# Performance work log

Hardware: AMD Instinct MI355X
Metric: run time of the kernel (lower is better)

The kernel has to match this reference:

```python
import jax, jax.numpy as jnp
import numpy as np

DIM = 192
K_LARGE = 21
K_SMALL = 5
EPS = 1e-5
DN = ('NCHW', 'OIHW', 'NCHW')


def depthwise_conv(x, w, k):
    pad = k // 2
    return jax.lax.conv_general_dilated(
        x, w, window_strides=(1, 1), padding=[(pad, pad), (pad, pad)],
        dimension_numbers=DN, feature_group_count=DIM)


def setup_inputs() -> dict:
    key = jax.random.key(0)
    ks = jax.random.split(key, 7)
    x = jax.random.normal(ks[0], (16, DIM, 56, 56), dtype=jnp.float32)
    w_large = jax.random.normal(ks[1], (DIM, 1, K_LARGE, K_LARGE), dtype=jnp.float32) * 0.05
    w_small = jax.random.normal(ks[2], (DIM, 1, K_SMALL, K_SMALL), dtype=jnp.float32) * 0.1
    gamma = jnp.ones((DIM,), dtype=jnp.float32)
    beta = jnp.zeros((DIM,), dtype=jnp.float32)
    w_pw = jax.random.normal(ks[3], (DIM, DIM, 1, 1), dtype=jnp.float32) * 0.05
    b_pw = jnp.zeros((DIM,), dtype=jnp.float32)
    return {"x": x, "w_large": w_large, "w_small": w_small,
            "gamma": gamma, "beta": beta, "w_pw": w_pw, "b_pw": b_pw}


def reference(x, w_large, w_small, gamma, beta, w_pw, b_pw):
    identity = x
    out = depthwise_conv(x, w_large, K_LARGE) + depthwise_conv(x, w_small, K_SMALL)
    # GroupNorm with 1 group: normalize over (C,H,W) per sample
    mean = jnp.mean(out, axis=(1, 2, 3), keepdims=True)
    var = jnp.var(out, axis=(1, 2, 3), keepdims=True)
    out = (out - mean) * jax.lax.rsqrt(var + EPS)
    out = out * gamma[None, :, None, None] + beta[None, :, None, None]
    out = jax.nn.gelu(out, approximate=False)  # torch nn.GELU default is exact
    # 1x1 pointwise conv with bias
    out = jax.lax.conv_general_dilated(
        out, w_pw, window_strides=(1, 1), padding='VALID', dimension_numbers=DN)
    out = out + b_pw[None, :, None, None]
    return out + identity
```

## Files before the change

### kernel.cpp

```cpp
#include <hip/hip_runtime.h>
#include <math.h>

#define DIM 192
#define HW 56
#define NPIX 3136
#define NSAMP 16
#define GN_EPS 1e-5f

typedef float f32x2 __attribute__((ext_vector_type(2)));
typedef float f32x4 __attribute__((ext_vector_type(4)));
typedef float f32x16 __attribute__((ext_vector_type(16)));
typedef unsigned int u32x4 __attribute__((ext_vector_type(4)));
typedef _Float16 h2 __attribute__((ext_vector_type(2)));
typedef _Float16 h8 __attribute__((ext_vector_type(8)));
typedef __bf16 bf16x8 __attribute__((ext_vector_type(8)));

#define WS_OFF_PARTIALS 38535168
#define WS_OFF_STATS    38559744
#define WS_OFF_WB       38559872

__device__ __forceinline__ unsigned int pack_h2(float a, float b) {
    h2 h;
    h[0] = (_Float16)a;
    h[1] = (_Float16)b;
    return __builtin_bit_cast(unsigned int, h);
}

__global__ void conv_w_kernel(const float* __restrict__ w, __bf16* __restrict__ wb) {
    int i = blockIdx.x * 256 + threadIdx.x;
    if (i < DIM * DIM) wb[i] = (__bf16)w[i];
}

#define S2(PH, t) ((((PH) - (t)) % 21 + 21) % 21)
#define AB16(a, b) __builtin_amdgcn_alignbit((a), (b), 16)

#define RING_Q(rg, dd, PH, QMAX) do { \
    rg[S2(PH,0)] += dd[0]; \
    rg[S2(PH,1)] += dd[1]; \
    rg[S2(PH,2)] += dd[2]; \
    rg[S2(PH,3)] += dd[3]; \
    if (12 <= (QMAX)) rg[S2(PH,8)]  += dd[4]; else rg[S2(PH,8)]  += hi ? 0.f : dd[4]; \
    if (13 <= (QMAX)) rg[S2(PH,9)]  += dd[5]; else rg[S2(PH,9)]  += hi ? 0.f : dd[5]; \
    if (14 <= (QMAX)) rg[S2(PH,10)] += dd[6]; else rg[S2(PH,10)] += hi ? 0.f : dd[6]; \
    if (15 <= (QMAX)) rg[S2(PH,11)] += dd[7]; \
    else if (11 <= (QMAX)) rg[S2(PH,11)] += hi ? 0.f : dd[7]; \
    if (20 <= (QMAX)) rg[S2(PH,16)] += dd[8]; \
    else if (16 <= (QMAX)) rg[S2(PH,16)] += hi ? 0.f : dd[8]; \
    if (17 <= (QMAX)) rg[S2(PH,17)] += hi ? 0.f : dd[9]; \
    rg[S2(PH,4)] += hi ? dd[9] : 0.f; \
    if (18 <= (QMAX)) rg[S2(PH,18)] += hi ? 0.f : dd[10]; \
    rg[S2(PH,5)] += hi ? dd[10] : 0.f; \
    if (19 <= (QMAX)) rg[S2(PH,19)] += hi ? 0.f : dd[11]; \
    rg[S2(PH,6)] += hi ? dd[11] : 0.f; \
    if (11 <= (QMAX)) rg[S2(PH,11)] += hi ? 0.f : dd[12]; \
    if (12 <= (QMAX)) rg[S2(PH,12)] += hi ? 0.f : dd[13]; \
} while (0)

#define STEP(PH_, QMAX_, RVAL_) do { \
    const unsigned int* rp = base + ((RVAL_) - 10) * 48; \
    unsigned int d0 = rp[0], d1 = rp[1], d2 = rp[2], d3 = rp[3], d4 = rp[4]; \
    unsigned int e0 = rp[8], e1 = rp[9], e2 = rp[10], e3 = rp[11], e4 = rp[12]; \
    { \
        u32x4 q0; q0[0] = d0; q0[1] = d1; q0[2] = d2; q0[3] = d3; \
        u32x4 q1; q1[0] = e0; q1[1] = e1; q1[2] = e2; q1[3] = e3; \
        f32x16 acc = __builtin_amdgcn_mfma_f32_32x32x16_f16( \
            A0, __builtin_bit_cast(h8, q0), CZ, 0, 0, 0); \
        acc = __builtin_amdgcn_mfma_f32_32x32x16_f16( \
            A1, __builtin_bit_cast(h8, q1), acc, 0, 0, 0); \
        RING_Q(ring0, acc, PH_, QMAX_); \
    } \
    { \
        u32x4 q0, q1; \
        q0[0] = AB16(d1, d0); q0[1] = AB16(d2, d1); q0[2] = AB16(d3, d2); q0[3] = AB16(d4, d3); \
        q1[0] = AB16(e1, e0); q1[1] = AB16(e2, e1); q1[2] = AB16(e3, e2); q1[3] = AB16(e4, e3); \
        f32x16 acc = __builtin_amdgcn_mfma_f32_32x32x16_f16( \
            A0, __builtin_bit_cast(h8, q0), CZ, 0, 0, 0); \
        acc = __builtin_amdgcn_mfma_f32_32x32x16_f16( \
            A1, __builtin_bit_cast(h8, q1), acc, 0, 0, 0); \
        RING_Q(ring1, acc, PH_, QMAX_); \
    } \
} while (0)

#define EMIT(PH_, RVAL_) do { \
    const int s0 = S2(PH_, 20), s1 = S2(PH_, 16); \
    float p0 = hi ? ring0[s1] : ring0[s0]; \
    float p1 = hi ? ring1[s1] : ring1[s0]; \
    ring0[s0] = hi ? ring0[s0] : 0.f; \
    ring0[s1] = hi ? 0.f : ring0[s1]; \
    ring1[s0] = hi ? ring1[s0] : 0.f; \
    ring1[s1] = hi ? 0.f : ring1[s1]; \
    float t0 = p0 + __shfl_xor(p0, 32); \
    float t1 = p1 + __shfl_xor(p1, 32); \
    if (!hi && nok) { \
        const int y = (RVAL_) - 20; \
        f32x2 st; st[0] = t0; st[1] = t1; \
        *(f32x2*)(top + y * HW + 2 * n) = st; \
        lsum += t0 + t1; \
        lss += t0 * t0 + t1 * t1; \
    } \
} while (0)

__global__ __launch_bounds__(64, 3)
void dwconv_kernel(const float* __restrict__ x,
                   const float* __restrict__ wl,
                   const float* __restrict__ wsm,
                   float* __restrict__ tmp,
                   float* __restrict__ partials) {
    __shared__ unsigned int tile[56 * 48];

    const int plane = blockIdx.x;
    const int ch = plane % DIM;
    const int l = threadIdx.x;
    const int n = l & 31;
    const int h = l >> 5;
    const bool hi = (h == 1);
    const bool nok = (n < 28);
    const float* xp = x + (size_t)plane * NPIX;

    {
        u32x4* t4 = (u32x4*)tile;
        for (int i = l; i < 672; i += 64) {
            u32x4 z; z[0] = 0; z[1] = 0; z[2] = 0; z[3] = 0;
            t4[i] = z;
        }
    }
    __syncthreads();
    for (int i = l; i < 56 * 28; i += 64) {
        int row = i / 28, j = i - row * 28;
        f32x2 v = *(const f32x2*)(xp + row * HW + 2 * j);
        tile[row * 48 + 5 + j] = pack_h2(v[0], v[1]);
    }

    h8 A0, A1;
    {
        const int m = n;
        #pragma unroll
        for (int e = 0; e < 8; ++e) {
            int tp = 8 * h + e;
            float v0 = 0.f, v1 = 0.f;
            if (m <= 20) {
                if (tp <= 20) v0 = wl[ch * 441 + m * 21 + tp];
                int tq = tp + 16;
                if (tq <= 20) v1 = wl[ch * 441 + m * 21 + tq];
            } else if (m <= 25 && tp >= 8 && tp <= 12) {
                v0 = wsm[ch * 25 + (m - 21) * 5 + (tp - 8)];
            }
            A0[e] = (_Float16)v0;
            A1[e] = (_Float16)v1;
        }
    }
    __syncthreads();

    float ring0[21], ring1[21];
    #pragma unroll
    for (int s = 0; s < 21; ++s) { ring0[s] = 0.f; ring1[s] = 0.f; }
    f32x16 CZ;
    #pragma unroll
    for (int s = 0; s < 16; ++s) CZ[s] = 0.f;

    float lsum = 0.f, lss = 0.f;
    float* top = tmp + (size_t)plane * NPIX;
    const unsigned int* base = tile + (n + 4 * h);

    #pragma unroll
    for (int rr = 0; rr < 10; ++rr) {
        STEP(10 + rr, 10 + rr, 10 + rr);
    }
    for (int bb = 0; bb < 3; ++bb) {
        #pragma unroll
        for (int u = 0; u < 21; ++u) {
            const int r = 20 + 21 * bb + u;
            if (r > 75) continue;
            if (r < 66) {
                STEP(20 + u, 20, r);
            }
            EMIT(20 + u, r);
        }
    }

    #pragma unroll
    for (int off = 32; off > 0; off >>= 1) {
        lsum += __shfl_down(lsum, off);
        lss  += __shfl_down(lss, off);
    }
    if (l == 0) {
        partials[2 * plane + 0] = lsum;
        partials[2 * plane + 1] = lss;
    }
}

__global__ void stats_kernel(const float* __restrict__ partials, float* __restrict__ stats) {
    const int n = blockIdx.x;
    const int t = threadIdx.x;
    float s = 0.f, ss = 0.f;
    for (int c = t; c < DIM; c += 64) {
        s  += partials[2 * (n * DIM + c) + 0];
        ss += partials[2 * (n * DIM + c) + 1];
    }
    #pragma unroll
    for (int off = 32; off > 0; off >>= 1) {
        s  += __shfl_down(s, off);
        ss += __shfl_down(ss, off);
    }
    if (t == 0) {
        const float inv = 1.f / 602112.f;
        float mean = s * inv;
        float var = ss * inv - mean * mean;
        stats[2 * n + 0] = mean;
        stats[2 * n + 1] = rsqrtf(var + GN_EPS);
    }
}

__device__ __forceinline__ float fast_gelu(float y) {
    float z = fabsf(y) * 0.70710678118654752f;
    float tt = __builtin_amdgcn_rcpf(1.f + 0.3275911f * z);
    float poly = tt * (0.254829592f + tt * (-0.284496736f + tt * (1.421413741f
               + tt * (-1.453152027f + tt * 1.061405429f))));
    float er = 1.f - poly * __expf(-z * z);
    er = copysignf(er, y);
    return 0.5f * y * (1.f + er);
}

__global__ __launch_bounds__(192)
void pw_kernel(const float* __restrict__ tmp, const float* __restrict__ x,
               const float* __restrict__ gamma, const float* __restrict__ beta,
               const __bf16* __restrict__ wb, const float* __restrict__ bpw,
               const float* __restrict__ stats, float* __restrict__ out) {
    __shared__ __bf16 g_lds[32 * 200];

    const int bid = blockIdx.x;
    const int n = bid / 98;
    const int pt = bid - n * 98;
    const int px0 = pt * 32;
    const int t = threadIdx.x;

    const float mean = stats[2 * n + 0];
    const float rstd = stats[2 * n + 1];

    {
        const float a = rstd * gamma[t];
        const float b = beta[t] - mean * a;
        const float* tp = tmp + ((size_t)n * DIM + t) * NPIX + px0;
        #pragma unroll
        for (int k = 0; k < 8; ++k) {
            f32x4 v = *(const f32x4*)(tp + 4 * k);
            #pragma unroll
            for (int j = 0; j < 4; ++j) {
                float y = v[j] * a + b;
                g_lds[(4 * k + j) * 200 + t] = (__bf16)fast_gelu(y);
            }
        }
    }
    __syncthreads();

    const int w = t >> 6;
    const int l = t & 63;
    const int lane16 = l & 15, lg = l >> 4;

    f32x4 acc[2][4];
    #pragma unroll
    for (int p = 0; p < 2; ++p)
        #pragma unroll
        for (int m = 0; m < 4; ++m) { acc[p][m][0]=0.f; acc[p][m][1]=0.f; acc[p][m][2]=0.f; acc[p][m][3]=0.f; }

    const char* gbase = (const char*)g_lds;
    #pragma unroll
    for (int kk = 0; kk < 6; ++kk) {
        const int k0 = 32 * kk;
        bf16x8 bf0 = *(const bf16x8*)(gbase + lane16 * 400 + (k0 + 8 * lg) * 2);
        bf16x8 bf1 = *(const bf16x8*)(gbase + (16 + lane16) * 400 + (k0 + 8 * lg) * 2);
        #pragma unroll
        for (int m = 0; m < 4; ++m) {
            const int co = 64 * w + 16 * m + lane16;
            bf16x8 af = *(const bf16x8*)(wb + co * DIM + k0 + 8 * lg);
            acc[0][m] = __builtin_amdgcn_mfma_f32_16x16x32_bf16(af, bf0, acc[0][m], 0, 0, 0);
            acc[1][m] = __builtin_amdgcn_mfma_f32_16x16x32_bf16(af, bf1, acc[1][m], 0, 0, 0);
        }
    }

    const float* xb = x + (size_t)n * DIM * NPIX;
    float* ob = out + (size_t)n * DIM * NPIX;
    #pragma unroll
    for (int m = 0; m < 4; ++m) {
        f32x4 b4 = *(const f32x4*)(bpw + 64 * w + 16 * m + 4 * lg);
        #pragma unroll
        for (int p = 0; p < 2; ++p)
            #pragma unroll
            for (int j = 0; j < 4; ++j) {
                const int co = 64 * w + 16 * m + 4 * lg + j;
                const int idx = co * NPIX + px0 + p * 16 + lane16;
                ob[idx] = acc[p][m][j] + b4[j] + xb[idx];
            }
    }
}

extern "C" void kernel_launch(void* const* d_in, const int* in_sizes, int n_in,
                              void* d_out, int out_size, void* d_ws, size_t ws_size,
                              hipStream_t stream) {
    (void)in_sizes; (void)n_in; (void)out_size; (void)ws_size;
    const float* x     = (const float*)d_in[0];
    const float* wl    = (const float*)d_in[1];
    const float* wsm   = (const float*)d_in[2];
    const float* gamma = (const float*)d_in[3];
    const float* beta  = (const float*)d_in[4];
    const float* wpw   = (const float*)d_in[5];
    const float* bpw   = (const float*)d_in[6];
    float* out = (float*)d_out;

    char* wsb = (char*)d_ws;
    float* tmp      = (float*)wsb;
    float* partials = (float*)(wsb + WS_OFF_PARTIALS);
    float* stats    = (float*)(wsb + WS_OFF_STATS);
    __bf16* wb      = (__bf16*)(wsb + WS_OFF_WB);

    conv_w_kernel<<<144, 256, 0, stream>>>(wpw, wb);
    dwconv_kernel<<<NSAMP * DIM, 64, 0, stream>>>(x, wl, wsm, tmp, partials);
    stats_kernel<<<NSAMP, 64, 0, stream>>>(partials, stats);
    pw_kernel<<<NSAMP * 98, 192, 0, stream>>>(tmp, x, gamma, beta, wb, bpw, stats, out);
}
```

Before: 114.4 us.

## Vectorize LDS tile loads, use mask multiplies, pkrtz packing, relax launch bounds

Measured after the change: 126.4 us. +10.5%, slower.

```diff
diff --git a/kernel.cpp b/kernel.cpp
--- a/kernel.cpp
+++ b/kernel.cpp
@@ -13,6 +13,7 @@
 typedef unsigned int u32x4 __attribute__((ext_vector_type(4)));
 typedef _Float16 h2 __attribute__((ext_vector_type(2)));
 typedef _Float16 h8 __attribute__((ext_vector_type(8)));
+typedef __fp16 fp16x2 __attribute__((ext_vector_type(2)));
 typedef __bf16 bf16x8 __attribute__((ext_vector_type(8)));
 
 #define WS_OFF_PARTIALS 38535168
@@ -20,10 +21,8 @@
 #define WS_OFF_WB       38559872
 
 __device__ __forceinline__ unsigned int pack_h2(float a, float b) {
-    h2 h;
-    h[0] = (_Float16)a;
-    h[1] = (_Float16)b;
-    return __builtin_bit_cast(unsigned int, h);
+    fp16x2 r = __builtin_amdgcn_cvt_pkrtz(a, b);
+    return __builtin_bit_cast(unsigned int, r);
 }
 
 __global__ void conv_w_kernel(const float* __restrict__ w, __bf16* __restrict__ wb) {
@@ -39,40 +38,41 @@
     rg[S2(PH,1)] += dd[1]; \
     rg[S2(PH,2)] += dd[2]; \
     rg[S2(PH,3)] += dd[3]; \
-    if (12 <= (QMAX)) rg[S2(PH,8)]  += dd[4]; else rg[S2(PH,8)]  += hi ? 0.f : dd[4]; \
-    if (13 <= (QMAX)) rg[S2(PH,9)]  += dd[5]; else rg[S2(PH,9)]  += hi ? 0.f : dd[5]; \
-    if (14 <= (QMAX)) rg[S2(PH,10)] += dd[6]; else rg[S2(PH,10)] += hi ? 0.f : dd[6]; \
+    if (12 <= (QMAX)) rg[S2(PH,8)]  += dd[4];  else rg[S2(PH,8)]  += mlo * dd[4]; \
+    if (13 <= (QMAX)) rg[S2(PH,9)]  += dd[5];  else rg[S2(PH,9)]  += mlo * dd[5]; \
+    if (14 <= (QMAX)) rg[S2(PH,10)] += dd[6];  else rg[S2(PH,10)] += mlo * dd[6]; \
     if (15 <= (QMAX)) rg[S2(PH,11)] += dd[7]; \
-    else if (11 <= (QMAX)) rg[S2(PH,11)] += hi ? 0.f : dd[7]; \
+    else if (11 <= (QMAX)) rg[S2(PH,11)] += mlo * dd[7]; \
     if (20 <= (QMAX)) rg[S2(PH,16)] += dd[8]; \
-    else if (16 <= (QMAX)) rg[S2(PH,16)] += hi ? 0.f : dd[8]; \
-    if (17 <= (QMAX)) rg[S2(PH,17)] += hi ? 0.f : dd[9]; \
-    rg[S2(PH,4)] += hi ? dd[9] : 0.f; \
-    if (18 <= (QMAX)) rg[S2(PH,18)] += hi ? 0.f : dd[10]; \
-    rg[S2(PH,5)] += hi ? dd[10] : 0.f; \
-    if (19 <= (QMAX)) rg[S2(PH,19)] += hi ? 0.f : dd[11]; \
-    rg[S2(PH,6)] += hi ? dd[11] : 0.f; \
-    if (11 <= (QMAX)) rg[S2(PH,11)] += hi ? 0.f : dd[12]; \
-    if (12 <= (QMAX)) rg[S2(PH,12)] += hi ? 0.f : dd[13]; \
+    else if (16 <= (QMAX)) rg[S2(PH,16)] += mlo * dd[8]; \
+    if (17 <= (QMAX)) rg[S2(PH,17)] += mlo * dd[9]; \
+    rg[S2(PH,4)] += mhi * dd[9]; \
+    if (18 <= (QMAX)) rg[S2(PH,18)] += mlo * dd[10]; \
+    rg[S2(PH,5)] += mhi * dd[10]; \
+    if (19 <= (QMAX)) rg[S2(PH,19)] += mlo * dd[11]; \
+    rg[S2(PH,6)] += mhi * dd[11]; \
+    if (11 <= (QMAX)) rg[S2(PH,11)] += mlo * dd[12]; \
+    if (12 <= (QMAX)) rg[S2(PH,12)] += mlo * dd[13]; \
 } while (0)
 
 #define STEP(PH_, QMAX_, RVAL_) do { \
     const unsigned int* rp = base + ((RVAL_) - 10) * 48; \
-    unsigned int d0 = rp[0], d1 = rp[1], d2 = rp[2], d3 = rp[3], d4 = rp[4]; \
-    unsigned int e0 = rp[8], e1 = rp[9], e2 = rp[10], e3 = rp[11], e4 = rp[12]; \
+    u32x4 dq = *(const u32x4*)rp; \
+    unsigned int d4 = rp[4]; \
+    u32x4 eq = *(const u32x4*)(rp + 8); \
     { \
-        u32x4 q0; q0[0] = d0; q0[1] = d1; q0[2] = d2; q0[3] = d3; \
-        u32x4 q1; q1[0] = e0; q1[1] = e1; q1[2] = e2; q1[3] = e3; \
         f32x16 acc = __builtin_amdgcn_mfma_f32_32x32x16_f16( \
-            A0, __builtin_bit_cast(h8, q0), CZ, 0, 0, 0); \
+            A0, __builtin_bit_cast(h8, dq), CZ, 0, 0, 0); \
         acc = __builtin_amdgcn_mfma_f32_32x32x16_f16( \
-            A1, __builtin_bit_cast(h8, q1), acc, 0, 0, 0); \
+            A1, __builtin_bit_cast(h8, eq), acc, 0, 0, 0); \
         RING_Q(ring0, acc, PH_, QMAX_); \
     } \
     { \
         u32x4 q0, q1; \
-        q0[0] = AB16(d1, d0); q0[1] = AB16(d2, d1); q0[2] = AB16(d3, d2); q0[3] = AB16(d4, d3); \
-        q1[0] = AB16(e1, e0); q1[1] = AB16(e2, e1); q1[2] = AB16(e3, e2); q1[3] = AB16(e4, e3); \
+        q0[0] = AB16(dq[1], dq[0]); q0[1] = AB16(dq[2], dq[1]); \
+        q0[2] = AB16(dq[3], dq[2]); q0[3] = AB16(d4, dq[3]); \
+        q1[0] = AB16(eq[1], eq[0]); q1[1] = AB16(eq[2], eq[1]); \
+        q1[2] = AB16(eq[3], eq[2]); q1[3] = q1[2];  \
         f32x16 acc = __builtin_amdgcn_mfma_f32_32x32x16_f16( \
             A0, __builtin_bit_cast(h8, q0), CZ, 0, 0, 0); \
         acc = __builtin_amdgcn_mfma_f32_32x32x16_f16( \
@@ -85,10 +85,10 @@
     const int s0 = S2(PH_, 20), s1 = S2(PH_, 16); \
     float p0 = hi ? ring0[s1] : ring0[s0]; \
     float p1 = hi ? ring1[s1] : ring1[s0]; \
-    ring0[s0] = hi ? ring0[s0] : 0.f; \
-    ring0[s1] = hi ? 0.f : ring0[s1]; \
-    ring1[s0] = hi ? ring1[s0] : 0.f; \
-    ring1[s1] = hi ? 0.f : ring1[s1]; \
+    ring0[s0] *= mhi;   \
+    ring0[s1] *= mlo;   \
+    ring1[s0] *= mhi; \
+    ring1[s1] *= mlo; \
     float t0 = p0 + __shfl_xor(p0, 32); \
     float t1 = p1 + __shfl_xor(p1, 32); \
     if (!hi && nok) { \
@@ -100,7 +100,7 @@
     } \
 } while (0)
 
-__global__ __launch_bounds__(64, 3)
+__global__ __launch_bounds__(64, 2)
 void dwconv_kernel(const float* __restrict__ x,
                    const float* __restrict__ wl,
                    const float* __restrict__ wsm,
@@ -115,6 +115,8 @@
     const int h = l >> 5;
     const bool hi = (h == 1);
     const bool nok = (n < 28);
+    const float mlo = hi ? 0.f : 1.f;
+    const float mhi = hi ? 1.f : 0.f;
     const float* xp = x + (size_t)plane * NPIX;
 
     {
```
